# Performance work log

Hardware: AMD Instinct MI355X
Metric: run time of the kernel (lower is better)

The kernel has to match this reference:

```python
import jax, jax.numpy as jnp
import numpy as np

D_MODEL = 1024
NUM_HEADS = 16
D_K = D_MODEL // NUM_HEADS


def setup_inputs() -> dict:
    key = jax.random.key(0)
    ks = jax.random.split(key, 5)
    B, S = 4, 2048
    scale = 1.0 / np.sqrt(D_MODEL)
    x = jax.random.normal(ks[0], (B, S, D_MODEL), dtype=jnp.float32)
    # Linear(d_model, d_model, bias=False) weights, stored as [out, in] like torch
    Wq = jax.random.normal(ks[1], (D_MODEL, D_MODEL), dtype=jnp.float32) * scale
    Wk = jax.random.normal(ks[2], (D_MODEL, D_MODEL), dtype=jnp.float32) * scale
    Wv = jax.random.normal(ks[3], (D_MODEL, D_MODEL), dtype=jnp.float32) * scale
    Wo = jax.random.normal(ks[4], (D_MODEL, D_MODEL), dtype=jnp.float32) * scale
    return {"x": x, "Wq": Wq, "Wk": Wk, "Wv": Wv, "Wo": Wo}


def reference(x, Wq, Wk, Wv, Wo):
    B, S, D = x.shape
    H, dk = NUM_HEADS, D_K
    # projections (torch Linear: x @ W.T)
    q = (x @ Wq.T).reshape(B, S, H, dk).transpose(0, 2, 1, 3)  # [B,H,S,dk]
    k = (x @ Wk.T).reshape(B, S, H, dk).transpose(0, 2, 1, 3)
    v = (x @ Wv.T).reshape(B, S, H, dk).transpose(0, 2, 1, 3)
    scores = jnp.einsum("bhqd,bhkd->bhqk", q, k) / jnp.sqrt(jnp.float32(dk))
    causal = jnp.triu(jnp.ones((S, S), dtype=bool), k=1)  # True above diagonal -> masked
    scores = jnp.where(causal[None, None], -jnp.inf, scores)
    attn = jax.nn.softmax(scores, axis=-1)
    out = jnp.einsum("bhqk,bhkd->bhqd", attn, v)  # [B,H,S,dk]
    out = out.transpose(0, 2, 1, 3).reshape(B, S, D)
    return out @ Wo.T
```

## Files before the change

### kernel.cpp

```cpp
#include <hip/hip_runtime.h>

typedef __bf16 bf16_t;
typedef __bf16 bf16x8 __attribute__((ext_vector_type(8)));
typedef __bf16 bf16x4 __attribute__((ext_vector_type(4)));
typedef float f32x4 __attribute__((ext_vector_type(4)));
typedef unsigned short u16x8 __attribute__((ext_vector_type(8)));

#define AS1C(p) ((const __attribute__((address_space(1))) void*)(p))
#define AS3(p) ((__attribute__((address_space(3))) void*)(p))

__device__ __forceinline__ unsigned short f2b_rne(float f) {
  union { float f; unsigned u; } x; x.f = f;
  unsigned u = x.u;
  u += 0x7fffu + ((u >> 16) & 1u);
  return (unsigned short)(u >> 16);
}

__device__ __forceinline__ float fast_exp2(float x) {
  return __builtin_amdgcn_exp2f(x);
}

__global__ __launch_bounds__(256) void cast_f32_bf16(const float* __restrict__ in,
                                                     unsigned short* __restrict__ out,
                                                     int n) {
  int i = (blockIdx.x * 256 + threadIdx.x) * 8;
  if (i >= n) return;
  const float4* p = reinterpret_cast<const float4*>(in + i);
  float4 a = p[0], b = p[1];
  u16x8 o;
  o[0] = f2b_rne(a.x); o[1] = f2b_rne(a.y); o[2] = f2b_rne(a.z); o[3] = f2b_rne(a.w);
  o[4] = f2b_rne(b.x); o[5] = f2b_rne(b.y); o[6] = f2b_rne(b.z); o[7] = f2b_rne(b.w);
  *reinterpret_cast<u16x8*>(out + i) = o;
}

__global__ __launch_bounds__(256) void cast_w4(const float* __restrict__ w0,
                                               const float* __restrict__ w1,
                                               const float* __restrict__ w2,
                                               const float* __restrict__ w3,
                                               unsigned short* __restrict__ out) {
  const float* in = (blockIdx.y == 0) ? w0 : (blockIdx.y == 1) ? w1
                  : (blockIdx.y == 2) ? w2 : w3;
  int i = (blockIdx.x * 256 + threadIdx.x) * 8;
  unsigned short* o = out + (size_t)blockIdx.y * (1024u * 1024u);
  const float4* p = reinterpret_cast<const float4*>(in + i);
  float4 a = p[0], b = p[1];
  u16x8 v;
  v[0] = f2b_rne(a.x); v[1] = f2b_rne(a.y); v[2] = f2b_rne(a.z); v[3] = f2b_rne(a.w);
  v[4] = f2b_rne(b.x); v[5] = f2b_rne(b.y); v[6] = f2b_rne(b.z); v[7] = f2b_rne(b.w);
  *reinterpret_cast<u16x8*>(o + i) = v;
}

template <int OUT_F32>
__global__ __launch_bounds__(256) void gemm_bt(const bf16_t* __restrict__ A,
                                               const bf16_t* __restrict__ Bm,
                                               void* __restrict__ C,
                                               int M, int N, int K, int lda,
                                               float scale, int qlim) {
  __shared__ bf16_t As[128 * 32];
  __shared__ bf16_t Bs[128 * 32];
  const int tid = threadIdx.x;
  const int lane = tid & 63, wave = tid >> 6;
  const int wm = wave >> 1, wn = wave & 1;
  const int r = lane & 15, kg = lane >> 4;
  const int m0 = blockIdx.y * 128, n0 = blockIdx.x * 128;
  const float sc = (n0 < qlim) ? scale : 1.0f;
  f32x4 acc[4][4] = {};
  const size_t abase = (size_t)m0 * lda;
  const size_t bbase = (size_t)n0 * K;
  for (int k0 = 0; k0 < K; k0 += 32) {
#pragma unroll
    for (int c = 0; c < 2; ++c) {
      int e = (c * 256 + tid) * 8;
      int rr = e >> 5, cc = e & 31;
      __builtin_amdgcn_global_load_lds(AS1C(A + abase + (size_t)rr * lda + k0 + cc),
                                       AS3(As + (c * 256 + wave * 64) * 8), 16, 0, 0);
      __builtin_amdgcn_global_load_lds(AS1C(Bm + bbase + (size_t)rr * K + k0 + cc),
                                       AS3(Bs + (c * 256 + wave * 64) * 8), 16, 0, 0);
    }
    __syncthreads();
    bf16x8 af[4], bfr[4];
#pragma unroll
    for (int t = 0; t < 4; ++t) {
      af[t]  = *reinterpret_cast<const bf16x8*>(As + (wm * 64 + t * 16 + r) * 32 + kg * 8);
      bfr[t] = *reinterpret_cast<const bf16x8*>(Bs + (wn * 64 + t * 16 + r) * 32 + kg * 8);
    }
    __builtin_amdgcn_s_setprio(1);
#pragma unroll
    for (int i = 0; i < 4; ++i)
#pragma unroll
      for (int j = 0; j < 4; ++j)
        acc[i][j] = __builtin_amdgcn_mfma_f32_16x16x32_bf16(af[i], bfr[j], acc[i][j], 0, 0, 0);
    __builtin_amdgcn_s_setprio(0);
    __syncthreads();
  }
#pragma unroll
  for (int i = 0; i < 4; ++i) {
#pragma unroll
    for (int j = 0; j < 4; ++j) {
      const int mb = m0 + wm * 64 + i * 16 + kg * 4;
      const int nc = n0 + wn * 64 + j * 16 + r;
#pragma unroll
      for (int v = 0; v < 4; ++v) {
        float val = acc[i][j][v] * sc;
        size_t idx = (size_t)(mb + v) * N + nc;
        if (OUT_F32) reinterpret_cast<float*>(C)[idx] = val;
        else reinterpret_cast<unsigned short*>(C)[idx] = f2b_rne(val);
      }
    }
  }
}

__global__ __launch_bounds__(256) void transpose_v(const bf16_t* __restrict__ qkv,
                                                   bf16_t* __restrict__ vt) {
  __shared__ bf16_t Vs[64 * 72];
  const int t = threadIdx.x;
  const int s0 = blockIdx.x * 64;
  const int bh = blockIdx.y;
  const int b = bh >> 4, h = bh & 15;
  const size_t in_base = ((size_t)b * 2048 + s0) * 3072 + 2048 + h * 64;
#pragma unroll
  for (int c = 0; c < 2; ++c) {
    int chunk = c * 256 + t;
    int ss = chunk >> 3, dd = (chunk & 7) * 8;
    bf16x8 v = *reinterpret_cast<const bf16x8*>(qkv + in_base + (size_t)ss * 3072 + dd);
    *reinterpret_cast<bf16x8*>(Vs + ss * 72 + dd) = v;
  }
  __syncthreads();
  const size_t out_base = (size_t)bh * 64 * 2048 + s0;
#pragma unroll
  for (int c = 0; c < 2; ++c) {
    int chunk = c * 256 + t;
    int dd = chunk >> 3, ss = (chunk & 7) * 8;
    bf16x8 o;
#pragma unroll
    for (int j = 0; j < 8; ++j) o[j] = Vs[(ss + j) * 72 + dd];
    *reinterpret_cast<bf16x8*>(vt + out_base + (size_t)dd * 2048 + ss) = o;
  }
}

__global__ __launch_bounds__(512) void flash_attn(const bf16_t* __restrict__ QKV,
                                                  const bf16_t* __restrict__ VT,
                                                  unsigned short* __restrict__ O,
                                                  int ostride) {
  __shared__ bf16_t Ks[2][64 * 72];
  __shared__ bf16_t Vts[2][64 * 72];
  __shared__ bf16_t Pl[8][16 * 72];
  const int tid = threadIdx.x;
  const int lane = tid & 63, wave = tid >> 6;
  const int r = lane & 15, kg = lane >> 4;
  const int bh = blockIdx.x;
  const int pair = blockIdx.y;
  const int b = bh >> 4, h = bh & 15;
  const size_t qkv_row0 = (size_t)b * 2048 * 3072;
  const int qcol = h * 64, kcol = 1024 + h * 64;
  const size_t vt_base = (size_t)bh * 64 * 2048;
  const size_t o_row0 = (size_t)b * 2048 * ostride;
  const int ocol = h * 64;
  const int srr = tid >> 3, scc = (tid & 7) * 8;

  for (int pass = 0; pass < 2; ++pass) {
    const int qt = pass ? (15 - pair) : pair;
    const int q0 = qt * 128;
    const int qrow = q0 + wave * 16 + r;
    const int tmax_w = (q0 + wave * 16 + 15) >> 6;
    const int ntiles = qt * 2 + 2;

    const size_t qoff = qkv_row0 + (size_t)qrow * 3072 + qcol;
    bf16x8 qf0 = *reinterpret_cast<const bf16x8*>(QKV + qoff + kg * 8);
    bf16x8 qf1 = *reinterpret_cast<const bf16x8*>(QKV + qoff + 32 + kg * 8);

    f32x4 oacc[4] = {};
    float m_run = -3e30f, l_lane = 0.f;

    bf16x8 gk = *reinterpret_cast<const bf16x8*>(QKV + qkv_row0 + (size_t)srr * 3072 + kcol + scc);
    bf16x8 gv = *reinterpret_cast<const bf16x8*>(VT + vt_base + (size_t)srr * 2048 + scc);

    for (int t = 0; t < ntiles; ++t) {
      const int buf = t & 1;
      *reinterpret_cast<bf16x8*>(&Ks[buf][srr * 72 + scc]) = gk;
      *reinterpret_cast<bf16x8*>(&Vts[buf][srr * 72 + scc]) = gv;
      __syncthreads();
      if (t + 1 < ntiles) {
        const int kv1 = (t + 1) * 64;
        gk = *reinterpret_cast<const bf16x8*>(QKV + qkv_row0 + (size_t)(kv1 + srr) * 3072 + kcol + scc);
        gv = *reinterpret_cast<const bf16x8*>(VT + vt_base + (size_t)srr * 2048 + kv1 + scc);
      }
      if (t > tmax_w) continue;

      const int kv0 = t * 64;
      float vals[16];
#pragma unroll
      for (int nt = 0; nt < 4; ++nt) {
        bf16x8 kf0 = *reinterpret_cast<const bf16x8*>(&Ks[buf][(nt * 16 + r) * 72 + kg * 8]);
        bf16x8 kf1 = *reinterpret_cast<const bf16x8*>(&Ks[buf][(nt * 16 + r) * 72 + 32 + kg * 8]);
        f32x4 s = {};
        __builtin_amdgcn_s_setprio(1);
        s = __builtin_amdgcn_mfma_f32_16x16x32_bf16(kf0, qf0, s, 0, 0, 0);
        s = __builtin_amdgcn_mfma_f32_16x16x32_bf16(kf1, qf1, s, 0, 0, 0);
        __builtin_amdgcn_s_setprio(0);
#pragma unroll
        for (int v = 0; v < 4; ++v) vals[nt * 4 + v] = s[v];
      }
      if (t == tmax_w) {
#pragma unroll
        for (int nt = 0; nt < 4; ++nt)
#pragma unroll
          for (int v = 0; v < 4; ++v)
            if (kv0 + nt * 16 + kg * 4 + v > qrow) vals[nt * 4 + v] = -3e30f;
      }
      float a0 = fmaxf(fmaxf(vals[0], vals[1]), vals[2]);
      float a1 = fmaxf(fmaxf(vals[3], vals[4]), vals[5]);
      float a2 = fmaxf(fmaxf(vals[6], vals[7]), vals[8]);
      float a3 = fmaxf(fmaxf(vals[9], vals[10]), vals[11]);
      float a4 = fmaxf(fmaxf(vals[12], vals[13]), vals[14]);
      float pmax = fmaxf(fmaxf(fmaxf(a0, a1), fmaxf(a2, a3)), fmaxf(a4, vals[15]));
      if (!__all(pmax <= m_run + 8.0f)) {
        pmax = fmaxf(pmax, __shfl_xor(pmax, 16));
        pmax = fmaxf(pmax, __shfl_xor(pmax, 32));
        const float m_new = fmaxf(m_run, pmax);
        const float alpha = fast_exp2(m_run - m_new);
        l_lane *= alpha;
        f32x4 al;
#pragma unroll
        for (int v = 0; v < 4; ++v) al[v] = __shfl(alpha, kg * 4 + v);
#pragma unroll
        for (int dt = 0; dt < 4; ++dt)
#pragma unroll
          for (int v = 0; v < 4; ++v) oacc[dt][v] *= al[v];
        m_run = m_new;
      }
#pragma unroll
      for (int ii = 0; ii < 16; ++ii) {
        float p = fast_exp2(vals[ii] - m_run);
        vals[ii] = p;
        l_lane += p;
      }

#pragma unroll
      for (int nt = 0; nt < 4; ++nt) {
        bf16x4 pb;
#pragma unroll
        for (int v = 0; v < 4; ++v) pb[v] = (bf16_t)vals[nt * 4 + v];
        *reinterpret_cast<bf16x4*>(&Pl[wave][r * 72 + nt * 16 + kg * 4]) = pb;
      }
      bf16x8 pa0 = *reinterpret_cast<const bf16x8*>(&Pl[wave][r * 72 + kg * 8]);
      bf16x8 pa1 = *reinterpret_cast<const bf16x8*>(&Pl[wave][r * 72 + 32 + kg * 8]);

#pragma unroll
      for (int dt = 0; dt < 4; ++dt) {
        bf16x8 vb0 = *reinterpret_cast<const bf16x8*>(&Vts[buf][(dt * 16 + r) * 72 + kg * 8]);
        bf16x8 vb1 = *reinterpret_cast<const bf16x8*>(&Vts[buf][(dt * 16 + r) * 72 + 32 + kg * 8]);
        __builtin_amdgcn_s_setprio(1);
        oacc[dt] = __builtin_amdgcn_mfma_f32_16x16x32_bf16(pa0, vb0, oacc[dt], 0, 0, 0);
        oacc[dt] = __builtin_amdgcn_mfma_f32_16x16x32_bf16(pa1, vb1, oacc[dt], 0, 0, 0);
        __builtin_amdgcn_s_setprio(0);
      }
    }

    float l_row = l_lane;
    l_row += __shfl_xor(l_row, 16);
    l_row += __shfl_xor(l_row, 32);
    const float linv = 1.0f / l_row;
    f32x4 il;
#pragma unroll
    for (int v = 0; v < 4; ++v) il[v] = __shfl(linv, kg * 4 + v);
    const size_t orow0 = o_row0 + (size_t)(q0 + wave * 16) * ostride + ocol;
#pragma unroll
    for (int dt = 0; dt < 4; ++dt) {
      const int d = dt * 16 + r;
#pragma unroll
      for (int v = 0; v < 4; ++v)
        O[orow0 + (size_t)(kg * 4 + v) * ostride + d] = f2b_rne(oacc[dt][v] * il[v]);
    }
  }
}

extern "C" void kernel_launch(void* const* d_in, const int* in_sizes, int n_in,
                              void* d_out, int out_size, void* d_ws, size_t ws_size,
                              hipStream_t stream) {
  const float* x  = (const float*)d_in[0];
  const float* Wq = (const float*)d_in[1];
  const float* Wk = (const float*)d_in[2];
  const float* Wv = (const float*)d_in[3];
  const float* Wo = (const float*)d_in[4];

  char* ws = (char*)d_ws;
  bf16_t* xb  = (bf16_t*)(ws);
  bf16_t* wqb = (bf16_t*)(ws + (16u << 20));
  bf16_t* wob = (bf16_t*)(ws + (22u << 20));
  bf16_t* qkv = (bf16_t*)(ws + (24u << 20));
  bf16_t* vt  = (bf16_t*)(ws);

  const int NX = 4 * 2048 * 1024;
  cast_f32_bf16<<<NX / 2048, 256, 0, stream>>>(x, (unsigned short*)xb, NX);
  cast_w4<<<dim3(512, 4), 256, 0, stream>>>(Wq, Wk, Wv, Wo, (unsigned short*)wqb);

  gemm_bt<0><<<dim3(3072 / 128, 8192 / 128), 256, 0, stream>>>(
      xb, wqb, qkv, 8192, 3072, 1024, 1024, 0.18033688011112042f, 1024);

  transpose_v<<<dim3(2048 / 64, 64), 256, 0, stream>>>(qkv, vt);

  flash_attn<<<dim3(64, 8), 512, 0, stream>>>(qkv, vt, (unsigned short*)qkv, 3072);

  gemm_bt<1><<<dim3(1024 / 128, 8192 / 128), 256, 0, stream>>>(
      qkv, wob, d_out, 8192, 1024, 1024, 3072, 1.0f, 0);
}
```

Baseline: 186.8 us.

## Replace projection GEMMs with 256x256 eight-wave pipelined GEMM using swizzled LDS

```diff
diff --git a/kernel.cpp b/kernel.cpp
--- a/kernel.cpp
+++ b/kernel.cpp
@@ -8,6 +8,7 @@
 
 #define AS1C(p) ((const __attribute__((address_space(1))) void*)(p))
 #define AS3(p) ((__attribute__((address_space(3))) void*)(p))
+#define MM(a, b, c) __builtin_amdgcn_mfma_f32_16x16x32_bf16(a, b, c, 0, 0, 0)
 
 __device__ __forceinline__ unsigned short f2b_rne(float f) {
   union { float f; unsigned u; } x; x.f = f;
@@ -84,13 +85,11 @@
       af[t]  = *reinterpret_cast<const bf16x8*>(As + (wm * 64 + t * 16 + r) * 32 + kg * 8);
       bfr[t] = *reinterpret_cast<const bf16x8*>(Bs + (wn * 64 + t * 16 + r) * 32 + kg * 8);
     }
-    __builtin_amdgcn_s_setprio(1);
 #pragma unroll
     for (int i = 0; i < 4; ++i)
 #pragma unroll
       for (int j = 0; j < 4; ++j)
-        acc[i][j] = __builtin_amdgcn_mfma_f32_16x16x32_bf16(af[i], bfr[j], acc[i][j], 0, 0, 0);
-    __builtin_amdgcn_s_setprio(0);
+        acc[i][j] = MM(af[i], bfr[j], acc[i][j]);
     __syncthreads();
   }
 #pragma unroll
@@ -108,6 +107,117 @@
       }
     }
   }
+}
+
+#define LDSA(bb, ih, il, kk) \
+  (*reinterpret_cast<const bf16x8*>(lds + (bb) * 32768 + (ih) * 8192 + aoff##il + acol##kk))
+#define LDSB(bb, jh, jl, kk) \
+  (*reinterpret_cast<const bf16x8*>(lds + (bb) * 32768 + (jh) * 8192 + boff##jl + acol##kk))
+#define STG_A(bb, ih, rd, kt) \
+  __builtin_amdgcn_global_load_lds( \
+      AS1C(aSrc + (size_t)((ih) * 128 + (rd) * 64) * lda + (kt) * 64), \
+      AS3(lds + (bb) * 32768 + ((ih) * 128 + (rd) * 64 + w8) * 64), 16, 0, 0)
+#define STG_B(bb, ih, rd, kt) \
+  __builtin_amdgcn_global_load_lds( \
+      AS1C(bSrc + (size_t)((ih) * 128 + (rd) * 64) * (size_t)K + (kt) * 64), \
+      AS3(lds + (bb) * 32768 + 16384 + ((ih) * 128 + (rd) * 64 + w8) * 64), 16, 0, 0)
+#define PHASE(bb, qa, qb, RDA, RDB, VMC, ...) do { \
+  if (RDA) { A00 = LDSA(bb, qa, 0, 0); A01 = LDSA(bb, qa, 0, 1); \
+             A10 = LDSA(bb, qa, 1, 0); A11 = LDSA(bb, qa, 1, 1); \
+             A20 = LDSA(bb, qa, 2, 0); A21 = LDSA(bb, qa, 2, 1); \
+             A30 = LDSA(bb, qa, 3, 0); A31 = LDSA(bb, qa, 3, 1); } \
+  if (RDB) { B00 = LDSB(bb, qb, 0, 0); B01 = LDSB(bb, qb, 0, 1); \
+             B10 = LDSB(bb, qb, 1, 0); B11 = LDSB(bb, qb, 1, 1); } \
+  __VA_ARGS__; \
+  if (VMC) asm volatile("s_waitcnt vmcnt(4)" ::: "memory"); \
+  __builtin_amdgcn_s_barrier(); \
+  asm volatile("s_waitcnt lgkmcnt(0)" ::: "memory"); \
+  __builtin_amdgcn_sched_barrier(0); \
+  __builtin_amdgcn_s_setprio(1); \
+  acc[qa][0][qb][0] = MM(A01, B01, MM(A00, B00, acc[qa][0][qb][0])); \
+  acc[qa][0][qb][1] = MM(A01, B11, MM(A00, B10, acc[qa][0][qb][1])); \
+  acc[qa][1][qb][0] = MM(A11, B01, MM(A10, B00, acc[qa][1][qb][0])); \
+  acc[qa][1][qb][1] = MM(A11, B11, MM(A10, B10, acc[qa][1][qb][1])); \
+  acc[qa][2][qb][0] = MM(A21, B01, MM(A20, B00, acc[qa][2][qb][0])); \
+  acc[qa][2][qb][1] = MM(A21, B11, MM(A20, B10, acc[qa][2][qb][1])); \
+  acc[qa][3][qb][0] = MM(A31, B01, MM(A30, B00, acc[qa][3][qb][0])); \
+  acc[qa][3][qb][1] = MM(A31, B11, MM(A30, B10, acc[qa][3][qb][1])); \
+  __builtin_amdgcn_s_setprio(0); \
+  __builtin_amdgcn_s_barrier(); \
+} while (0)
+
+template <int OUT_F32>
+__global__ __launch_bounds__(512, 2) void gemm8(const bf16_t* __restrict__ A,
+                                                const bf16_t* __restrict__ Bm,
+                                                void* __restrict__ C,
+                                                int M, int N, int K, int lda,
+                                                float scale, int qlim) {
+  extern __shared__ bf16_t lds[];
+  const int tid = threadIdx.x;
+  const int w = tid >> 6, l = tid & 63;
+  const int r = l & 15, kg = l >> 4;
+  const int wm64 = (w >> 2) * 64, wn32 = (w & 3) * 32;
+  const int w8 = w * 8;
+  const int rowoff = l >> 3;
+  const int colsw = ((l & 7) ^ (l >> 3)) * 8;
+  const int m0 = blockIdx.y * 256, n0 = blockIdx.x * 256;
+  const bf16_t* aSrc = A + (size_t)(m0 + w8 + rowoff) * lda + colsw;
+  const bf16_t* bSrc = Bm + (size_t)(n0 + w8 + rowoff) * K + colsw;
+  const int acol0 = (kg ^ (r & 7)) * 8;
+  const int acol1 = ((4 + kg) ^ (r & 7)) * 8;
+  const int aoff0 = (wm64 + r) * 64;
+  const int aoff1 = (wm64 + 16 + r) * 64;
+  const int aoff2 = (wm64 + 32 + r) * 64;
+  const int aoff3 = (wm64 + 48 + r) * 64;
+  const int boff0 = 16384 + (wn32 + r) * 64;
+  const int boff1 = 16384 + (wn32 + 16 + r) * 64;
+
+  f32x4 acc[2][4][2][2] = {};
+  bf16x8 A00, A01, A10, A11, A20, A21, A30, A31, B00, B01, B10, B11;
+
+  STG_A(0, 0, 0, 0); STG_A(0, 0, 1, 0); STG_A(0, 1, 0, 0); STG_A(0, 1, 1, 0);
+  STG_B(0, 0, 0, 0); STG_B(0, 0, 1, 0); STG_B(0, 1, 0, 0); STG_B(0, 1, 1, 0);
+  STG_A(1, 0, 0, 1); STG_A(1, 0, 1, 1); STG_B(1, 1, 0, 1); STG_B(1, 1, 1, 1);
+  asm volatile("s_waitcnt vmcnt(0)" ::: "memory");
+  __builtin_amdgcn_s_barrier();
+
+  const int NT = K >> 6;
+  const int NIT = K >> 7;
+  for (int n = 0; n < NIT; ++n) {
+    const int kB = 2 * n + 1;
+    const int ks2 = (2 * n + 2 < NT) ? 2 * n + 2 : 2 * n;
+    const int ks3 = (2 * n + 3 < NT) ? 2 * n + 3 : kB;
+    PHASE(0, 0, 0, 1, 1, 0, STG_A(1, 1, 0, kB); STG_A(1, 1, 1, kB);
+                            STG_B(1, 0, 0, kB); STG_B(1, 0, 1, kB));
+    PHASE(0, 0, 1, 0, 1, 0, (void)0);
+    PHASE(0, 1, 1, 1, 0, 0, STG_A(0, 0, 0, ks2); STG_A(0, 0, 1, ks2));
+    PHASE(0, 1, 0, 0, 1, 1, STG_B(0, 1, 0, ks2); STG_B(0, 1, 1, ks2));
+    PHASE(1, 0, 0, 1, 1, 0, STG_A(0, 1, 0, ks2); STG_A(0, 1, 1, ks2);
+                            STG_B(0, 0, 0, ks2); STG_B(0, 0, 1, ks2));
+    PHASE(1, 0, 1, 0, 1, 0, (void)0);
+    PHASE(1, 1, 1, 1, 0, 0, STG_A(1, 0, 0, ks3); STG_A(1, 0, 1, ks3));
+    PHASE(1, 1, 0, 0, 1, 1, STG_B(1, 1, 0, ks3); STG_B(1, 1, 1, ks3));
+  }
+
+#pragma unroll
+  for (int qa = 0; qa < 2; ++qa)
+#pragma unroll
+    for (int il = 0; il < 4; ++il)
+#pragma unroll
+      for (int qb = 0; qb < 2; ++qb)
+#pragma unroll
+        for (int jl = 0; jl < 2; ++jl) {
+          const int row0 = m0 + qa * 128 + wm64 + il * 16 + kg * 4;
+          const int col = n0 + qb * 128 + wn32 + jl * 16 + r;
+          const float sc = (col < qlim) ? scale : 1.0f;
+#pragma unroll
+          for (int v = 0; v < 4; ++v) {
+            float val = acc[qa][il][qb][jl][v] * sc;
+            size_t idx = (size_t)(row0 + v) * N + col;
+            if (OUT_F32) reinterpret_cast<float*>(C)[idx] = val;
+            else reinterpret_cast<unsigned short*>(C)[idx] = f2b_rne(val);
+          }
+        }
 }
 
 __global__ __launch_bounds__(256) void transpose_v(const bf16_t* __restrict__ qkv,
@@ -195,8 +305,8 @@
         bf16x8 kf1 = *reinterpret_cast<const bf16x8*>(&Ks[buf][(nt * 16 + r) * 72 + 32 + kg * 8]);
         f32x4 s = {};
         __builtin_amdgcn_s_setprio(1);
-        s = __builtin_amdgcn_mfma_f32_16x16x32_bf16(kf0, qf0, s, 0, 0, 0);
-        s = __builtin_amdgcn_mfma_f32_16x16x32_bf16(kf1, qf1, s, 0, 0, 0);
+        s = MM(kf0, qf0, s);
+        s = MM(kf1, qf1, s);
         __builtin_amdgcn_s_setprio(0);
 #pragma unroll
         for (int v = 0; v < 4; ++v) vals[nt * 4 + v] = s[v];
@@ -235,7 +345,6 @@
         vals[ii] = p;
         l_lane += p;
       }
-
 #pragma unroll
       for (int nt = 0; nt < 4; ++nt) {
         bf16x4 pb;
@@ -245,14 +354,13 @@
       }
       bf16x8 pa0 = *reinterpret_cast<const bf16x8*>(&Pl[wave][r * 72 + kg * 8]);
       bf16x8 pa1 = *reinterpret_cast<const bf16x8*>(&Pl[wave][r * 72 + 32 + kg * 8]);
-
 #pragma unroll
       for (int dt = 0; dt < 4; ++dt) {
         bf16x8 vb0 = *reinterpret_cast<const bf16x8*>(&Vts[buf][(dt * 16 + r) * 72 + kg * 8]);
         bf16x8 vb1 = *reinterpret_cast<const bf16x8*>(&Vts[buf][(dt * 16 + r) * 72 + 32 + kg * 8]);
         __builtin_amdgcn_s_setprio(1);
-        oacc[dt] = __builtin_amdgcn_mfma_f32_16x16x32_bf16(pa0, vb0, oacc[dt], 0, 0, 0);
-        oacc[dt] = __builtin_amdgcn_mfma_f32_16x16x32_bf16(pa1, vb1, oacc[dt], 0, 0, 0);
+        oacc[dt] = MM(pa0, vb0, oacc[dt]);
+        oacc[dt] = MM(pa1, vb1, oacc[dt]);
         __builtin_amdgcn_s_setprio(0);
       }
     }
@@ -291,17 +399,22 @@
   bf16_t* qkv = (bf16_t*)(ws + (24u << 20));
   bf16_t* vt  = (bf16_t*)(ws);
 
+  hipFuncSetAttribute(reinterpret_cast<const void*>(&gemm8<0>),
+                      hipFuncAttributeMaxDynamicSharedMemorySize, 131072);
+  hipFuncSetAttribute(reinterpret_cast<const void*>(&gemm8<1>),
+                      hipFuncAttributeMaxDynamicSharedMemorySize, 131072);
+
   const int NX = 4 * 2048 * 1024;
   cast_f32_bf16<<<NX / 2048, 256, 0, stream>>>(x, (unsigned short*)xb, NX);
   cast_w4<<<dim3(512, 4), 256, 0, stream>>>(Wq, Wk, Wv, Wo, (unsigned short*)wqb);
 
-  gemm_bt<0><<<dim3(3072 / 128, 8192 / 128), 256, 0, stream>>>(
+  gemm8<0><<<dim3(3072 / 256, 8192 / 256), 512, 131072, stream>>>(
       xb, wqb, qkv, 8192, 3072, 1024, 1024, 0.18033688011112042f, 1024);
 
   transpose_v<<<dim3(2048 / 64, 64), 256, 0, stream>>>(qkv, vt);
 
   flash_attn<<<dim3(64, 8), 512, 0, stream>>>(qkv, vt, (unsigned short*)qkv, 3072);
 
-  gemm_bt<1><<<dim3(1024 / 128, 8192 / 128), 256, 0, stream>>>(
+  gemm8<1><<<dim3(1024 / 256, 8192 / 256), 512, 131072, stream>>>(
       qkv, wob, d_out, 8192, 1024, 1024, 3072, 1.0f, 0);
 }
```

Result: faster. 182.9 us (-2.1%).

## Rewrite projection GEMMs with triple-buffered LDS pipeline and swizzled 128x256 tiles

Applied to the files above, without the earlier changes.

```diff
diff --git a/kernel.cpp b/kernel.cpp
--- a/kernel.cpp
+++ b/kernel.cpp
@@ -8,6 +8,7 @@
 
 #define AS1C(p) ((const __attribute__((address_space(1))) void*)(p))
 #define AS3(p) ((__attribute__((address_space(3))) void*)(p))
+#define MM(a, b, c) __builtin_amdgcn_mfma_f32_16x16x32_bf16(a, b, c, 0, 0, 0)
 
 __device__ __forceinline__ unsigned short f2b_rne(float f) {
   union { float f; unsigned u; } x; x.f = f;
@@ -51,63 +52,104 @@
 }
 
 template <int OUT_F32>
-__global__ __launch_bounds__(256) void gemm_bt(const bf16_t* __restrict__ A,
-                                               const bf16_t* __restrict__ Bm,
-                                               void* __restrict__ C,
-                                               int M, int N, int K, int lda,
-                                               float scale, int qlim) {
-  __shared__ bf16_t As[128 * 32];
-  __shared__ bf16_t Bs[128 * 32];
+__global__ __launch_bounds__(512, 2) void gemm4(const bf16_t* __restrict__ A,
+                                                const bf16_t* __restrict__ Bm,
+                                                void* __restrict__ C,
+                                                int M, int N, int K, int lda,
+                                                float scale, int qlim) {
+  extern __shared__ bf16_t lds[];
   const int tid = threadIdx.x;
-  const int lane = tid & 63, wave = tid >> 6;
-  const int wm = wave >> 1, wn = wave & 1;
-  const int r = lane & 15, kg = lane >> 4;
-  const int m0 = blockIdx.y * 128, n0 = blockIdx.x * 128;
-  const float sc = (n0 < qlim) ? scale : 1.0f;
-  f32x4 acc[4][4] = {};
-  const size_t abase = (size_t)m0 * lda;
-  const size_t bbase = (size_t)n0 * K;
-  for (int k0 = 0; k0 < K; k0 += 32) {
-#pragma unroll
-    for (int c = 0; c < 2; ++c) {
-      int e = (c * 256 + tid) * 8;
-      int rr = e >> 5, cc = e & 31;
-      __builtin_amdgcn_global_load_lds(AS1C(A + abase + (size_t)rr * lda + k0 + cc),
-                                       AS3(As + (c * 256 + wave * 64) * 8), 16, 0, 0);
-      __builtin_amdgcn_global_load_lds(AS1C(Bm + bbase + (size_t)rr * K + k0 + cc),
-                                       AS3(Bs + (c * 256 + wave * 64) * 8), 16, 0, 0);
+  const int w = tid >> 6, l = tid & 63;
+  const int r = l & 15, kg = l >> 4;
+  const int wm64 = (w >> 2) * 64, wn32 = (w & 3) * 32;
+  const int w8 = w * 8;
+  const int m0 = blockIdx.y * 128, n0 = blockIdx.x * 256;
+  const bf16_t* aSrc = A + (size_t)(m0 + w8 + (l >> 3)) * lda + ((l & 7) ^ (l >> 3)) * 8;
+  const bf16_t* bSrc = Bm + (size_t)(n0 + w8 + (l >> 3)) * K + ((l & 7) ^ (l >> 3)) * 8;
+  const int acol0 = (kg ^ (r & 7)) * 8;
+  const int acol1 = ((4 + kg) ^ (r & 7)) * 8;
+
+  f32x4 acc[2][4][2] = {};
+
+  auto STAGE = [&](bf16_t* sb, int kt) {
+    const bf16_t* ak = aSrc + kt * 64;
+    const bf16_t* bk = bSrc + kt * 64;
+    __builtin_amdgcn_global_load_lds(AS1C(ak),                    AS3(sb + (w8) * 64), 16, 0, 0);
+    __builtin_amdgcn_global_load_lds(AS1C(ak + (size_t)64 * lda), AS3(sb + (64 + w8) * 64), 16, 0, 0);
+    __builtin_amdgcn_global_load_lds(AS1C(bk),                    AS3(sb + 8192 + (w8) * 64), 16, 0, 0);
+    __builtin_amdgcn_global_load_lds(AS1C(bk + (size_t)64 * K),   AS3(sb + 8192 + (64 + w8) * 64), 16, 0, 0);
+    __builtin_amdgcn_global_load_lds(AS1C(bk + (size_t)128 * K),  AS3(sb + 8192 + (128 + w8) * 64), 16, 0, 0);
+    __builtin_amdgcn_global_load_lds(AS1C(bk + (size_t)192 * K),  AS3(sb + 8192 + (192 + w8) * 64), 16, 0, 0);
+  };
+
+  bf16_t* cur = lds;
+  bf16_t* nxt = lds + 24576;
+  bf16_t* stg = lds + 49152;
+
+  STAGE(cur, 0);
+  STAGE(nxt, 1);
+  asm volatile("s_waitcnt vmcnt(6)" ::: "memory");
+  __builtin_amdgcn_s_barrier();
+
+  const int NT = K >> 6;
+  for (int t = 0; t < NT; ++t) {
+    bf16x8 AF[4][2], BF[2][2][2];
+#pragma unroll
+    for (int il = 0; il < 4; ++il) {
+      const int ao = (wm64 + il * 16 + r) * 64;
+      AF[il][0] = *reinterpret_cast<const bf16x8*>(cur + ao + acol0);
+      AF[il][1] = *reinterpret_cast<const bf16x8*>(cur + ao + acol1);
     }
-    __syncthreads();
-    bf16x8 af[4], bfr[4];
-#pragma unroll
-    for (int t = 0; t < 4; ++t) {
-      af[t]  = *reinterpret_cast<const bf16x8*>(As + (wm * 64 + t * 16 + r) * 32 + kg * 8);
-      bfr[t] = *reinterpret_cast<const bf16x8*>(Bs + (wn * 64 + t * 16 + r) * 32 + kg * 8);
-    }
+#pragma unroll
+    for (int qb = 0; qb < 2; ++qb)
+#pragma unroll
+      for (int jl = 0; jl < 2; ++jl) {
+        const int bo = 8192 + (qb * 128 + wn32 + jl * 16 + r) * 64;
+        BF[qb][jl][0] = *reinterpret_cast<const bf16x8*>(cur + bo + acol0);
+        BF[qb][jl][1] = *reinterpret_cast<const bf16x8*>(cur + bo + acol1);
+      }
+    const int kt = (t + 2 < NT) ? t + 2 : t;
+    STAGE(stg, kt);
+    asm volatile("s_waitcnt lgkmcnt(4)" ::: "memory");
+    __builtin_amdgcn_sched_barrier(0);
     __builtin_amdgcn_s_setprio(1);
 #pragma unroll
-    for (int i = 0; i < 4; ++i)
-#pragma unroll
-      for (int j = 0; j < 4; ++j)
-        acc[i][j] = __builtin_amdgcn_mfma_f32_16x16x32_bf16(af[i], bfr[j], acc[i][j], 0, 0, 0);
+    for (int il = 0; il < 4; ++il)
+#pragma unroll
+      for (int jl = 0; jl < 2; ++jl)
+        acc[0][il][jl] = MM(AF[il][1], BF[0][jl][1], MM(AF[il][0], BF[0][jl][0], acc[0][il][jl]));
     __builtin_amdgcn_s_setprio(0);
-    __syncthreads();
+    asm volatile("s_waitcnt lgkmcnt(0)" ::: "memory");
+    __builtin_amdgcn_sched_barrier(0);
+    __builtin_amdgcn_s_setprio(1);
+#pragma unroll
+    for (int il = 0; il < 4; ++il)
+#pragma unroll
+      for (int jl = 0; jl < 2; ++jl)
+        acc[1][il][jl] = MM(AF[il][1], BF[1][jl][1], MM(AF[il][0], BF[1][jl][0], acc[1][il][jl]));
+    __builtin_amdgcn_s_setprio(0);
+    asm volatile("s_waitcnt vmcnt(6)" ::: "memory");
+    __builtin_amdgcn_s_barrier();
+    bf16_t* tmp = cur; cur = nxt; nxt = stg; stg = tmp;
   }
-#pragma unroll
-  for (int i = 0; i < 4; ++i) {
-#pragma unroll
-    for (int j = 0; j < 4; ++j) {
-      const int mb = m0 + wm * 64 + i * 16 + kg * 4;
-      const int nc = n0 + wn * 64 + j * 16 + r;
-#pragma unroll
-      for (int v = 0; v < 4; ++v) {
-        float val = acc[i][j][v] * sc;
-        size_t idx = (size_t)(mb + v) * N + nc;
-        if (OUT_F32) reinterpret_cast<float*>(C)[idx] = val;
-        else reinterpret_cast<unsigned short*>(C)[idx] = f2b_rne(val);
-      }
-    }
-  }
+
+#pragma unroll
+  for (int qb = 0; qb < 2; ++qb)
+#pragma unroll
+    for (int il = 0; il < 4; ++il)
+#pragma unroll
+      for (int jl = 0; jl < 2; ++jl) {
+        const int row0 = m0 + wm64 + il * 16 + kg * 4;
+        const int col = n0 + qb * 128 + wn32 + jl * 16 + r;
+        const float sc = (col < qlim) ? scale : 1.0f;
+#pragma unroll
+        for (int v = 0; v < 4; ++v) {
+          float val = acc[qb][il][jl][v] * sc;
+          size_t idx = (size_t)(row0 + v) * N + col;
+          if (OUT_F32) reinterpret_cast<float*>(C)[idx] = val;
+          else reinterpret_cast<unsigned short*>(C)[idx] = f2b_rne(val);
+        }
+      }
 }
 
 __global__ __launch_bounds__(256) void transpose_v(const bf16_t* __restrict__ qkv,
@@ -195,8 +237,8 @@
         bf16x8 kf1 = *reinterpret_cast<const bf16x8*>(&Ks[buf][(nt * 16 + r) * 72 + 32 + kg * 8]);
         f32x4 s = {};
         __builtin_amdgcn_s_setprio(1);
-        s = __builtin_amdgcn_mfma_f32_16x16x32_bf16(kf0, qf0, s, 0, 0, 0);
-        s = __builtin_amdgcn_mfma_f32_16x16x32_bf16(kf1, qf1, s, 0, 0, 0);
+        s = MM(kf0, qf0, s);
+        s = MM(kf1, qf1, s);
         __builtin_amdgcn_s_setprio(0);
 #pragma unroll
         for (int v = 0; v < 4; ++v) vals[nt * 4 + v] = s[v];
@@ -235,7 +277,6 @@
         vals[ii] = p;
         l_lane += p;
       }
-
 #pragma unroll
       for (int nt = 0; nt < 4; ++nt) {
         bf16x4 pb;
@@ -245,14 +286,13 @@
       }
       bf16x8 pa0 = *reinterpret_cast<const bf16x8*>(&Pl[wave][r * 72 + kg * 8]);
       bf16x8 pa1 = *reinterpret_cast<const bf16x8*>(&Pl[wave][r * 72 + 32 + kg * 8]);
-
 #pragma unroll
       for (int dt = 0; dt < 4; ++dt) {
         bf16x8 vb0 = *reinterpret_cast<const bf16x8*>(&Vts[buf][(dt * 16 + r) * 72 + kg * 8]);
         bf16x8 vb1 = *reinterpret_cast<const bf16x8*>(&Vts[buf][(dt * 16 + r) * 72 + 32 + kg * 8]);
         __builtin_amdgcn_s_setprio(1);
-        oacc[dt] = __builtin_amdgcn_mfma_f32_16x16x32_bf16(pa0, vb0, oacc[dt], 0, 0, 0);
-        oacc[dt] = __builtin_amdgcn_mfma_f32_16x16x32_bf16(pa1, vb1, oacc[dt], 0, 0, 0);
+        oacc[dt] = MM(pa0, vb0, oacc[dt]);
+        oacc[dt] = MM(pa1, vb1, oacc[dt]);
         __builtin_amdgcn_s_setprio(0);
       }
     }
@@ -291,17 +331,22 @@
   bf16_t* qkv = (bf16_t*)(ws + (24u << 20));
   bf16_t* vt  = (bf16_t*)(ws);
 
+  hipFuncSetAttribute(reinterpret_cast<const void*>(&gemm4<0>),
+                      hipFuncAttributeMaxDynamicSharedMemorySize, 147456);
+  hipFuncSetAttribute(reinterpret_cast<const void*>(&gemm4<1>),
+                      hipFuncAttributeMaxDynamicSharedMemorySize, 147456);
+
   const int NX = 4 * 2048 * 1024;
   cast_f32_bf16<<<NX / 2048, 256, 0, stream>>>(x, (unsigned short*)xb, NX);
   cast_w4<<<dim3(512, 4), 256, 0, stream>>>(Wq, Wk, Wv, Wo, (unsigned short*)wqb);
 
-  gemm_bt<0><<<dim3(3072 / 128, 8192 / 128), 256, 0, stream>>>(
+  gemm4<0><<<dim3(3072 / 256, 8192 / 128), 512, 147456, stream>>>(
       xb, wqb, qkv, 8192, 3072, 1024, 1024, 0.18033688011112042f, 1024);
 
   transpose_v<<<dim3(2048 / 64, 64), 256, 0, stream>>>(qkv, vt);
 
   flash_attn<<<dim3(64, 8), 512, 0, stream>>>(qkv, vt, (unsigned short*)qkv, 3072);
 
-  gemm_bt<1><<<dim3(1024 / 128, 8192 / 128), 256, 0, stream>>>(
+  gemm4<1><<<dim3(1024 / 256, 8192 / 128), 512, 147456, stream>>>(
       qkv, wob, d_out, 8192, 1024, 1024, 3072, 1.0f, 0);
 }
```

Measured after the change: 184.6 us. Within noise of the previous version (-1.2%).
